# Kernel optimization log

Measured on AMD Instinct MI355X. Metric: run time of the kernel, lower is better.

The kernel has to match this reference:

```python
import jax, jax.numpy as jnp
import numpy as np

NUM_LAYERS = 4
HIDDEN = 64
IN_CH = 3
OUT_CH = 1


def setup_inputs() -> dict:
    key = jax.random.key(0)
    ks = jax.random.split(key, 16)
    s = 0.1  # weight init scale
    x = jax.random.normal(ks[0], (2, 64, 64, IN_CH), dtype=jnp.float32)
    lift_w = jax.random.normal(ks[1], (IN_CH, HIDDEN), dtype=jnp.float32) * s
    lift_b = jax.random.normal(ks[2], (HIDDEN,), dtype=jnp.float32) * s
    blk_w = jax.random.normal(ks[3], (NUM_LAYERS, HIDDEN, HIDDEN), dtype=jnp.float32) * s
    blk_b = jax.random.normal(ks[4], (NUM_LAYERS, HIDDEN), dtype=jnp.float32) * s
    q_w = jax.random.normal(ks[5], (NUM_LAYERS, HIDDEN, HIDDEN), dtype=jnp.float32) * s
    q_b = jax.random.normal(ks[6], (NUM_LAYERS, HIDDEN), dtype=jnp.float32) * s
    k_w = jax.random.normal(ks[7], (NUM_LAYERS, HIDDEN, HIDDEN), dtype=jnp.float32) * s
    k_b = jax.random.normal(ks[8], (NUM_LAYERS, HIDDEN), dtype=jnp.float32) * s
    v_w = jax.random.normal(ks[9], (NUM_LAYERS, HIDDEN, HIDDEN), dtype=jnp.float32) * s
    v_b = jax.random.normal(ks[10], (NUM_LAYERS, HIDDEN), dtype=jnp.float32) * s
    proj_w = jax.random.normal(ks[11], (HIDDEN, OUT_CH), dtype=jnp.float32) * s
    proj_b = jax.random.normal(ks[12], (OUT_CH,), dtype=jnp.float32) * s
    return {"x": x, "lift_w": lift_w, "lift_b": lift_b,
            "blk_w": blk_w, "blk_b": blk_b,
            "q_w": q_w, "q_b": q_b, "k_w": k_w, "k_b": k_b,
            "v_w": v_w, "v_b": v_b, "proj_w": proj_w, "proj_b": proj_b}


def reference(x, lift_w, lift_b, blk_w, blk_b, q_w, q_b, k_w, k_b, v_w, v_b, proj_w, proj_b):
    prefix = x.shape[:-1]           # (B, H, W)
    B = x.shape[0]
    xf = x.reshape(B, -1, x.shape[-1])   # [B, N, in_ch]
    N = xf.shape[1]
    h = xf @ lift_w + lift_b             # [B, N, d]
    d = h.shape[-1]
    scale = 1.0 / jnp.sqrt(jnp.float32(d))
    for i in range(NUM_LAYERS):
        q = h @ q_w[i] + q_b[i]
        k = h @ k_w[i] + k_b[i]
        v = h @ v_w[i] + v_b[i]
        # full dense kernel, as in torch.bmm(q, k^T)/sqrt(d)
        kern = jnp.einsum('bnd,bmd->bnm', q, k) * scale     # [B, N, N]
        integral = jnp.einsum('bnm,bmd->bnd', kern, v) / N  # [B, N, d]
        wh = h @ blk_w[i] + blk_b[i]
        h = jax.nn.gelu(wh + integral, approximate=False)   # torch F.gelu default = exact erf
    out = h @ proj_w + proj_b                               # [B, N, out_ch]
    return out.reshape(*prefix, out.shape[-1])
```

## Files before the change

### kernel.cpp

```cpp
#include <hip/hip_runtime.h>
#include <hip/hip_bf16.h>
#include <math.h>


#define NLAYER 4
#define NB 2
#define NN 4096
#define DD 64
#define RPB 32
#define NT 256
#define NBLK 256
#define SHP 68
#define C0F (1.0f/32768.0f)
#define PSZ 2304
#define NCH 128
#define CHW 18

typedef __hip_bfloat16 bf16;
typedef unsigned long long u64t;

__device__ __forceinline__ float b2f(const bf16 v) { return __bfloat162float(v); }

template <typename T> struct Acc;
template <> struct Acc<float> {
    static __device__ __forceinline__ float ld(const void* p, int i) { return ((const float*)p)[i]; }
    static __device__ __forceinline__ void st(void* p, int i, float v) { ((float*)p)[i] = v; }
};
template <> struct Acc<bf16> {
    static __device__ __forceinline__ float ld(const void* p, int i) { return b2f(((const bf16*)p)[i]); }
    static __device__ __forceinline__ void st(void* p, int i, float v) { ((bf16*)p)[i] = __float2bfloat16(v); }
};

__device__ __forceinline__ float gelu_exact(float x) {
    return 0.5f * x * (1.0f + erff(x * 0.70710678118654752f));
}

__device__ __forceinline__ float2 ldc2(const float* p) {
    u64t v = __hip_atomic_load((const u64t*)p, __ATOMIC_RELAXED, __HIP_MEMORY_SCOPE_AGENT);
    float2 r;
    r.x = __uint_as_float((unsigned)v);
    r.y = __uint_as_float((unsigned)(v >> 32));
    return r;
}
__device__ __forceinline__ void stc2(float* p, float a, float b) {
    u64t v = ((u64t)__float_as_uint(b) << 32) | (u64t)__float_as_uint(a);
    __hip_atomic_store((u64t*)p, v, __ATOMIC_RELAXED, __HIP_MEMORY_SCOPE_AGENT);
}
__device__ __forceinline__ unsigned ldw(unsigned* p) {
    return __hip_atomic_load(p, __ATOMIC_RELAXED, __HIP_MEMORY_SCOPE_AGENT);
}
__device__ __forceinline__ void stw(unsigned* p, unsigned v) {
    __hip_atomic_store(p, v, __ATOMIC_RELAXED, __HIP_MEMORY_SCOPE_AGENT);
}
__device__ __forceinline__ void pollw(unsigned* p, unsigned ep) {
    int guard = 0;
    while (ldw(p) < ep && ++guard < (1 << 18)) __builtin_amdgcn_s_sleep(2);
}

__device__ __forceinline__ void mm4x4(float (&acc)[4][4],
    float4 L0, float4 L1, float4 L2, float4 L3,
    float4 R0, float4 R1, float4 R2, float4 R3)
{
    const float L[4][4] = {{L0.x,L0.y,L0.z,L0.w},{L1.x,L1.y,L1.z,L1.w},
                           {L2.x,L2.y,L2.z,L2.w},{L3.x,L3.y,L3.z,L3.w}};
    const float R[4][4] = {{R0.x,R0.y,R0.z,R0.w},{R1.x,R1.y,R1.z,R1.w},
                           {R2.x,R2.y,R2.z,R2.w},{R3.x,R3.y,R3.z,R3.w}};
    #pragma unroll
    for (int a = 0; a < 4; a++)
        #pragma unroll
        for (int k = 0; k < 4; k++)
            #pragma unroll
            for (int b = 0; b < 4; b++)
                acc[a][b] += L[a][k] * R[k][b];
}

__device__ __forceinline__ void mmNT4x4(float (&acc)[4][4],
    float4 L0, float4 L1, float4 L2, float4 L3,
    float4 R0, float4 R1, float4 R2, float4 R3)
{
    const float L[4][4] = {{L0.x,L0.y,L0.z,L0.w},{L1.x,L1.y,L1.z,L1.w},
                           {L2.x,L2.y,L2.z,L2.w},{L3.x,L3.y,L3.z,L3.w}};
    const float R[4][4] = {{R0.x,R0.y,R0.z,R0.w},{R1.x,R1.y,R1.z,R1.w},
                           {R2.x,R2.y,R2.z,R2.w},{R3.x,R3.y,R3.z,R3.w}};
    #pragma unroll
    for (int a = 0; a < 4; a++)
        #pragma unroll
        for (int b = 0; b < 4; b++)
            #pragma unroll
            for (int k = 0; k < 4; k++)
                acc[a][b] += L[a][k] * R[b][k];
}

__device__ __forceinline__ void outer4x4(float (&acc)[4][4], float4 A, float4 B)
{
    const float Aa[4] = {A.x, A.y, A.z, A.w};
    const float Ba[4] = {B.x, B.y, B.z, B.w};
    #pragma unroll
    for (int a = 0; a < 4; a++)
        #pragma unroll
        for (int b = 0; b < 4; b++)
            acc[a][b] += Aa[a] * Ba[b];
}


#define SM_SS   23936
#define SM_SU   24000
#define SM_BK   24064
#define SM_BQ   24128
#define SM_BV   24192
#define SM_BE   24256
#define SM_QK   24320
#define SM_KQ   24384
#define SM_QBK  24448
#define SM_RED  24512
#define SM_TOT  24768

template <typename T>
__device__ void run_net(
    const void* x, const void* lw, const void* lb,
    const void* blkw, const void* blkb,
    const void* qw, const void* qb, const void* kw, const void* kb,
    const void* vw, const void* vb, const void* pw, const void* pb,
    void* out, float* Gpart, float* Gg,
    unsigned* aflag, unsigned* cflag,
    float* smem, int blk, int t)
{
    float (*sH)[SHP] = (float(*)[SHP])(smem);
    float (*B1)[SHP] = (float(*)[SHP])(smem + 2176);
    float (*B2)[SHP] = (float(*)[SHP])(smem + 6528);
    float (*B3)[SHP] = (float(*)[SHP])(smem + 10880);
    float (*B4)[SHP] = (float(*)[SHP])(smem + 15232);
    float (*B5)[SHP] = (float(*)[SHP])(smem + 19584);
    float* PS  = smem + 10880;
    float* RED = smem + 10880;
    float* sS  = smem + SM_SS;
    float* suS = smem + SM_SU;
    float* bkS = smem + SM_BK;
    float* bqS = smem + SM_BQ;
    float* bvS = smem + SM_BV;
    float* beS = smem + SM_BE;
    float* qkS = smem + SM_QK;
    float* kqS = smem + SM_KQ;
    float* qbkS = smem + SM_QBK;
    float (*red)[DD] = (float(*)[DD])(smem + SM_RED);

    const int row0 = blk * RPB;
    const int bb = blk >> 7;
    const int r = t >> 4, c4 = (t & 15) << 2;
    const int i4 = t >> 4, j4 = t & 15;
    const int r0 = i4 << 2, c0 = j4 << 2;

    #pragma unroll
    for (int a = 0; a < 2; a++) {
        const int row = r + 16 * a, gr = row0 + row;
        float x0 = Acc<T>::ld(x, gr * 3 + 0);
        float x1 = Acc<T>::ld(x, gr * 3 + 1);
        float x2 = Acc<T>::ld(x, gr * 3 + 2);
        float o[4];
        #pragma unroll
        for (int b = 0; b < 4; b++) {
            int c = c4 + b;
            o[b] = Acc<T>::ld(lb, c) + x0 * Acc<T>::ld(lw, c)
                 + x1 * Acc<T>::ld(lw, DD + c) + x2 * Acc<T>::ld(lw, 2 * DD + c);
        }
        *(float4*)&sH[row][c4] = make_float4(o[0], o[1], o[2], o[3]);
    }
    __syncthreads();

    for (int layer = 0; layer < NLAYER; layer++) {
        const unsigned ep = (unsigned)(layer + 1);
        float* GgL = Gg + (size_t)(layer * NB + bb) * PSZ;
        const int wOff = layer * DD * DD, bOff = layer * DD;

        {
            if (i4 <= j4) {
                float m[4][4];
                #pragma unroll
                for (int a = 0; a < 4; a++)
                    #pragma unroll
                    for (int b = 0; b < 4; b++) m[a][b] = 0.f;
                #pragma unroll 8
                for (int n = 0; n < RPB; n++)
                    outer4x4(m, *(const float4*)&sH[n][r0], *(const float4*)&sH[n][c0]);
                float* dst = PS + (i4 * (33 - i4) / 2 + (j4 - i4)) * 16;
                #pragma unroll
                for (int a = 0; a < 4; a++)
                    #pragma unroll
                    for (int b = 0; b < 4; b++) dst[a * 4 + b] = m[a][b];
            }
            if (t < DD) {
                float ss = 0.f;
                #pragma unroll 8
                for (int n = 0; n < RPB; n++) ss += sH[n][t];
                PS[2176 + t] = ss;
                PS[2240 + t] = 0.f;
            }
        }
        __syncthreads();
        {
            float* slot = Gpart + (size_t)blk * PSZ;
            #pragma unroll
            for (int k2 = 0; k2 < 4; k2++) {
                const int idx = 2 * (t + k2 * NT);
                stc2(&slot[idx], PS[idx], PS[idx + 1]);
            }
            if (t < 128) {
                const int idx = 2 * (t + 4 * NT);
                stc2(&slot[idx], PS[idx], PS[idx + 1]);
            }
        }
        __syncthreads();
        if (t == 0) stw(&aflag[blk], ep);

        for (int i2 = t; i2 < DD * DD; i2 += NT) {
            B1[i2 >> 6][i2 & 63] = Acc<T>::ld(qw, wOff + i2);
            B4[i2 >> 6][i2 & 63] = Acc<T>::ld(kw, wOff + i2);
        }
        if (t < DD) {
            bkS[t] = Acc<T>::ld(kb, bOff + t);
            bqS[t] = Acc<T>::ld(qb, bOff + t);
            bvS[t] = Acc<T>::ld(vb, bOff + t);
        }

        {
            if (t < NCH) pollw(&aflag[bb * NCH + t], ep);
            __syncthreads();
            const int chunk = blk & (NCH - 1);
            if (t < 144) {
                const int g = t / 9, p2 = t % 9;
                const float* base = Gpart + (size_t)(bb * NCH + g * 8) * PSZ
                                  + chunk * CHW + 2 * p2;
                float ax = 0.f, ay = 0.f;
                #pragma unroll
                for (int s2 = 0; s2 < 8; s2++) {
                    float2 v = ldc2(base + (size_t)s2 * PSZ);
                    ax += v.x; ay += v.y;
                }
                RED[g * 20 + 2 * p2]     = ax;
                RED[g * 20 + 2 * p2 + 1] = ay;
            }
            __syncthreads();
            if (t < 9) {
                float s0 = 0.f, s1 = 0.f;
                #pragma unroll
                for (int g = 0; g < 16; g++) {
                    s0 += RED[g * 20 + 2 * t];
                    s1 += RED[g * 20 + 2 * t + 1];
                }
                stc2(&GgL[chunk * CHW + 2 * t], s0, s1);
            }
            __syncthreads();
            if (t == 0) stw(&cflag[blk], ep);
        }

        {
            float acc[4][4];
            #pragma unroll
            for (int a = 0; a < 4; a++)
                #pragma unroll
                for (int b = 0; b < 4; b++) acc[a][b] = 0.f;
            #pragma unroll 2
            for (int e = 0; e < DD; e += 4)
                mmNT4x4(acc,
                      *(const float4*)&B1[r0 + 0][e], *(const float4*)&B1[r0 + 1][e],
                      *(const float4*)&B1[r0 + 2][e], *(const float4*)&B1[r0 + 3][e],
                      *(const float4*)&B4[c0 + 0][e], *(const float4*)&B4[c0 + 1][e],
                      *(const float4*)&B4[c0 + 2][e], *(const float4*)&B4[c0 + 3][e]);
            #pragma unroll
            for (int a = 0; a < 4; a++)
                *(float4*)&B2[r0 + a][c0] = make_float4(acc[a][0], acc[a][1], acc[a][2], acc[a][3]);

            if (t < DD) {
                float u = 0.f;
                for (int e = 0; e < DD; e++) u += B1[t][e] * bkS[e];
                qkS[t] = u;
            } else if (t < 2 * DD) {
                const int rr = t - DD;
                float u = 0.f;
                for (int e = 0; e < DD; e++) u += B4[rr][e] * bqS[e];
                kqS[rr] = u;
            } else if (t == 2 * DD) {
                float u = 0.f;
                for (int e = 0; e < DD; e++) u += bqS[e] * bkS[e];
                qbkS[0] = u;
            }
        }
        __syncthreads();
        for (int i2 = t; i2 < DD * DD; i2 += NT) {
            B1[i2 >> 6][i2 & 63] = Acc<T>::ld(vw, wOff + i2);
            B4[i2 >> 6][i2 & 63] = Acc<T>::ld(blkw, wOff + i2);
        }

        {
            if (t < NCH) pollw(&cflag[bb * NCH + t], ep);
            __syncthreads();
            if (i4 <= j4) {
                const float* src = GgL + (i4 * (33 - i4) / 2 + (j4 - i4)) * 16;
                #pragma unroll
                for (int a = 0; a < 4; a++)
                    *(float4*)&B3[r0 + a][c0] = *(const float4*)&src[a * 4];
            } else {
                const float* src = GgL + (j4 * (33 - j4) / 2 + (i4 - j4)) * 16;
                #pragma unroll
                for (int a = 0; a < 4; a++)
                    #pragma unroll
                    for (int b = 0; b < 4; b++)
                        B3[r0 + a][c0 + b] = src[b * 4 + a];
            }
            if (t < DD) sS[t] = GgL[2176 + t];
            __syncthreads();
        }

        {
            float acc[4][4];
            #pragma unroll
            for (int a = 0; a < 4; a++)
                #pragma unroll
                for (int b = 0; b < 4; b++) acc[a][b] = sS[r0 + a] * bvS[c0 + b];
            #pragma unroll 2
            for (int e = 0; e < DD; e += 4)
                mm4x4(acc,
                      *(const float4*)&B3[r0 + 0][e], *(const float4*)&B3[r0 + 1][e],
                      *(const float4*)&B3[r0 + 2][e], *(const float4*)&B3[r0 + 3][e],
                      *(const float4*)&B1[e + 0][c0], *(const float4*)&B1[e + 1][c0],
                      *(const float4*)&B1[e + 2][c0], *(const float4*)&B1[e + 3][c0]);
            #pragma unroll
            for (int a = 0; a < 4; a++)
                *(float4*)&B5[r0 + a][c0] = make_float4(acc[a][0], acc[a][1], acc[a][2], acc[a][3]);
        }
        {
            const int c = t & 63, q = t >> 6;
            float u = 0.f;
            #pragma unroll
            for (int d2 = 0; d2 < 16; d2++) u += sS[q * 16 + d2] * B1[q * 16 + d2][c];
            red[q][c] = u;
        }
        __syncthreads();
        if (t < DD) suS[t] = red[0][t] + red[1][t] + red[2][t] + red[3][t] + (float)NN * bvS[t];
        __syncthreads();

        {
            float acc[4][4];
            #pragma unroll
            for (int a = 0; a < 4; a++)
                #pragma unroll
                for (int b = 0; b < 4; b++) acc[a][b] = qkS[r0 + a] * suS[c0 + b];
            #pragma unroll 2
            for (int e = 0; e < DD; e += 4)
                mm4x4(acc,
                      *(const float4*)&B2[r0 + 0][e], *(const float4*)&B2[r0 + 1][e],
                      *(const float4*)&B2[r0 + 2][e], *(const float4*)&B2[r0 + 3][e],
                      *(const float4*)&B5[e + 0][c0], *(const float4*)&B5[e + 1][c0],
                      *(const float4*)&B5[e + 2][c0], *(const float4*)&B5[e + 3][c0]);
            float wloc[4][4];
            #pragma unroll
            for (int a = 0; a < 4; a++)
                #pragma unroll
                for (int b = 0; b < 4; b++)
                    wloc[a][b] = B4[r0 + a][c0 + b] + C0F * acc[a][b];
            {
                const int c = t & 63, q = t >> 6;
                float u = 0.f;
                #pragma unroll
                for (int e2 = 0; e2 < 16; e2++) u += kqS[q * 16 + e2] * B5[q * 16 + e2][c];
                red[q][c] = u;
            }
            __syncthreads();
            #pragma unroll
            for (int a = 0; a < 4; a++)
                *(float4*)&B3[r0 + a][c0] = make_float4(wloc[a][0], wloc[a][1], wloc[a][2], wloc[a][3]);
            if (t < DD) beS[t] = Acc<T>::ld(blkb, bOff + t)
                               + C0F * (red[0][t] + red[1][t] + red[2][t] + red[3][t]
                                        + qbkS[0] * suS[t]);
        }
        __syncthreads();

        float o[2][4];
        #pragma unroll
        for (int a = 0; a < 2; a++) {
            const int row = r + 16 * a;
            float acc2[4];
            #pragma unroll
            for (int b = 0; b < 4; b++) acc2[b] = beS[c4 + b];
            for (int d = 0; d < DD; d++) {
                float hv = sH[row][d];
                float4 w4 = *(const float4*)&B3[d][c4];
                acc2[0] += hv * w4.x; acc2[1] += hv * w4.y;
                acc2[2] += hv * w4.z; acc2[3] += hv * w4.w;
            }
            #pragma unroll
            for (int b = 0; b < 4; b++) o[a][b] = gelu_exact(acc2[b]);
        }

        if (layer == NLAYER - 1) {
            float pbv = Acc<T>::ld(pb, 0);
            #pragma unroll
            for (int a = 0; a < 2; a++) {
                float p = 0.f;
                #pragma unroll
                for (int b = 0; b < 4; b++) p += o[a][b] * Acc<T>::ld(pw, c4 + b);
                p += __shfl_xor(p, 1);
                p += __shfl_xor(p, 2);
                p += __shfl_xor(p, 4);
                p += __shfl_xor(p, 8);
                if ((t & 15) == 0) Acc<T>::st(out, row0 + r + 16 * a, p + pbv);
            }
        } else {
            __syncthreads();
            #pragma unroll
            for (int a = 0; a < 2; a++)
                *(float4*)&sH[r + 16 * a][c4] =
                    make_float4(o[a][0], o[a][1], o[a][2], o[a][3]);
            __syncthreads();
        }
    }
}

__global__ __launch_bounds__(NT) void gno_kernel(
    const void* x, const void* lw, const void* lb,
    const void* blkw, const void* blkb,
    const void* qw, const void* qb, const void* kw, const void* kb,
    const void* vw, const void* vb, const void* pw, const void* pb,
    void* out, float* Gpart, float* Gg, unsigned* bar, int mode)
{
    __shared__ alignas(16) float smem[SM_TOT];
    __shared__ int stot;

    const int blk = blockIdx.x, t = threadIdx.x;

    bool isbf;
    if (mode >= 0) {
        isbf = (mode == 1);
    } else {
        if (t == 0) stot = 0;
        __syncthreads();
        int cdt = 0;
        const unsigned int* xw = (const unsigned int*)x;
        for (int i = t; i < 8192; i += NT) {
            unsigned u = xw[i] & 0xFFFFu;
            int e = (u >> 7) & 0xFF;
            cdt += (u == 0u || (e >= 100 && e <= 142)) ? 1 : 0;
        }
        atomicAdd(&stot, cdt);
        __syncthreads();
        isbf = (stot > 4915);
    }

    unsigned* aflag = bar;
    unsigned* cflag = bar + 256;

    if (isbf)
        run_net<bf16>(x, lw, lb, blkw, blkb, qw, qb, kw, kb, vw, vb, pw, pb,
                      out, Gpart, Gg, aflag, cflag, smem, blk, t);
    else
        run_net<float>(x, lw, lb, blkw, blkb, qw, qb, kw, kb, vw, vb, pw, pb,
                       out, Gpart, Gg, aflag, cflag, smem, blk, t);
}

extern "C" void kernel_launch(void* const* d_in, const int* in_sizes, int n_in,
                              void* d_out, int out_size, void* d_ws, size_t ws_size,
                              hipStream_t stream)
{
    const void* x    = d_in[0];
    const void* lw   = d_in[1];
    const void* lb   = d_in[2];
    const void* blkw = d_in[3];
    const void* blkb = d_in[4];
    const void* qw   = d_in[5];
    const void* qb   = d_in[6];
    const void* kw   = d_in[7];
    const void* kb   = d_in[8];
    const void* vw   = d_in[9];
    const void* vb   = d_in[10];
    const void* pw   = d_in[11];
    const void* pb   = d_in[12];

    int mode = -1;
    if (in_sizes && n_in > 0) {
        if (in_sizes[0] == 49152) mode = 1;
        else if (in_sizes[0] == 98304) mode = 0;
    }

    unsigned* bar = (unsigned*)d_ws;
    float* Gpart  = (float*)d_ws + 512;
    float* Gg     = Gpart + (size_t)NBLK * PSZ;

    (void)hipMemsetAsync(bar, 0, 512 * sizeof(unsigned), stream);
    gno_kernel<<<NBLK, NT, 0, stream>>>(x, lw, lb, blkw, blkb, qw, qb, kw, kb,
                                        vw, vb, pw, pb, d_out, Gpart, Gg, bar, mode);
}
```

Measured before the change: 158.1 us.

## Distribute Gram reduction by rows and fold V projection into per-row reduce

Each block now writes the full 64x64 Gram partial instead of the packed upper triangle. The cross-block reduction is reassigned so 65 blocks each reduce one row (or the column sums) and immediately multiply it by Wv. This removes the per-block 64x64x64 G·Wv matmul and the symmetric unpack, since every block then reads the finished G·Wv from global memory. In exchange it nearly doubles the partial-write traffic, leaves most blocks idle during the reduction, and moves the V weight load earlier.

```diff
diff --git a/kernel.cpp b/kernel.cpp
--- a/kernel.cpp
+++ b/kernel.cpp
@@ -12,9 +12,8 @@
 #define NBLK 256
 #define SHP 68
 #define C0F (1.0f/32768.0f)
-#define PSZ 2304
+#define PSZ 4160
 #define NCH 128
-#define CHW 18
 
 typedef __hip_bfloat16 bf16;
 typedef unsigned long long u64t;
@@ -146,6 +145,7 @@
 
     const int row0 = blk * RPB;
     const int bb = blk >> 7;
+    const int RC = blk & 127;
     const int r = t >> 4, c4 = (t & 15) << 2;
     const int i4 = t >> 4, j4 = t & 15;
     const int r0 = i4 << 2, c0 = j4 << 2;
@@ -173,39 +173,34 @@
         const int wOff = layer * DD * DD, bOff = layer * DD;
 
         {
-            if (i4 <= j4) {
-                float m[4][4];
-                #pragma unroll
-                for (int a = 0; a < 4; a++)
-                    #pragma unroll
-                    for (int b = 0; b < 4; b++) m[a][b] = 0.f;
-                #pragma unroll 8
-                for (int n = 0; n < RPB; n++)
-                    outer4x4(m, *(const float4*)&sH[n][r0], *(const float4*)&sH[n][c0]);
-                float* dst = PS + (i4 * (33 - i4) / 2 + (j4 - i4)) * 16;
-                #pragma unroll
-                for (int a = 0; a < 4; a++)
-                    #pragma unroll
-                    for (int b = 0; b < 4; b++) dst[a * 4 + b] = m[a][b];
-            }
+            float m[4][4];
+            #pragma unroll
+            for (int a = 0; a < 4; a++)
+                #pragma unroll
+                for (int b = 0; b < 4; b++) m[a][b] = 0.f;
+            #pragma unroll 8
+            for (int n = 0; n < RPB; n++)
+                outer4x4(m, *(const float4*)&sH[n][r0], *(const float4*)&sH[n][c0]);
+            #pragma unroll
+            for (int a = 0; a < 4; a++)
+                *(float4*)&PS[(r0 + a) * DD + c0] = make_float4(m[a][0], m[a][1], m[a][2], m[a][3]);
             if (t < DD) {
                 float ss = 0.f;
                 #pragma unroll 8
                 for (int n = 0; n < RPB; n++) ss += sH[n][t];
-                PS[2176 + t] = ss;
-                PS[2240 + t] = 0.f;
+                PS[4096 + t] = ss;
             }
         }
         __syncthreads();
         {
             float* slot = Gpart + (size_t)blk * PSZ;
             #pragma unroll
-            for (int k2 = 0; k2 < 4; k2++) {
+            for (int k2 = 0; k2 < 8; k2++) {
                 const int idx = 2 * (t + k2 * NT);
                 stc2(&slot[idx], PS[idx], PS[idx + 1]);
             }
-            if (t < 128) {
-                const int idx = 2 * (t + 4 * NT);
+            if (t < 32) {
+                const int idx = 2 * (t + 8 * NT);
                 stc2(&slot[idx], PS[idx], PS[idx + 1]);
             }
         }
@@ -215,6 +210,7 @@
         for (int i2 = t; i2 < DD * DD; i2 += NT) {
             B1[i2 >> 6][i2 & 63] = Acc<T>::ld(qw, wOff + i2);
             B4[i2 >> 6][i2 & 63] = Acc<T>::ld(kw, wOff + i2);
+            B5[i2 >> 6][i2 & 63] = Acc<T>::ld(vw, wOff + i2);
         }
         if (t < DD) {
             bkS[t] = Acc<T>::ld(kb, bOff + t);
@@ -222,36 +218,64 @@
             bvS[t] = Acc<T>::ld(vb, bOff + t);
         }
 
-        {
+        if (RC <= 64) {
             if (t < NCH) pollw(&aflag[bb * NCH + t], ep);
             __syncthreads();
-            const int chunk = blk & (NCH - 1);
-            if (t < 144) {
-                const int g = t / 9, p2 = t % 9;
-                const float* base = Gpart + (size_t)(bb * NCH + g * 8) * PSZ
-                                  + chunk * CHW + 2 * p2;
+            const int p2 = t & 31, g8 = t >> 5;
+            const int roff = (RC < 64) ? RC * DD : 4096;
+            {
+                const float* base = Gpart + (size_t)(bb * NCH + g8 * 16) * PSZ + roff + 2 * p2;
                 float ax = 0.f, ay = 0.f;
                 #pragma unroll
-                for (int s2 = 0; s2 < 8; s2++) {
+                for (int s2 = 0; s2 < 16; s2++) {
                     float2 v = ldc2(base + (size_t)s2 * PSZ);
                     ax += v.x; ay += v.y;
                 }
-                RED[g * 20 + 2 * p2]     = ax;
-                RED[g * 20 + 2 * p2 + 1] = ay;
-            }
-            __syncthreads();
-            if (t < 9) {
-                float s0 = 0.f, s1 = 0.f;
-                #pragma unroll
-                for (int g = 0; g < 16; g++) {
-                    s0 += RED[g * 20 + 2 * t];
-                    s1 += RED[g * 20 + 2 * t + 1];
+                RED[g8 * 64 + 2 * p2]     = ax;
+                RED[g8 * 64 + 2 * p2 + 1] = ay;
+            }
+            __syncthreads();
+            if (RC < 64) {
+                if (t < DD) {
+                    float u = 0.f;
+                    #pragma unroll
+                    for (int g = 0; g < 8; g++) u += RED[g * 64 + t];
+                    RED[512 + t] = u;
                 }
-                stc2(&GgL[chunk * CHW + 2 * t], s0, s1);
+                __syncthreads();
+                {
+                    const int c = t & 63, q4 = t >> 6;
+                    float u = 0.f;
+                    #pragma unroll
+                    for (int e2 = 0; e2 < 16; e2++)
+                        u += RED[512 + q4 * 16 + e2] * B5[q4 * 16 + e2][c];
+                    RED[576 + q4 * 64 + c] = u;
+                }
+                __syncthreads();
+                if (t < 32) {
+                    float v0 = 0.f, v1 = 0.f;
+                    #pragma unroll
+                    for (int q = 0; q < 4; q++) {
+                        v0 += RED[576 + q * 64 + 2 * t];
+                        v1 += RED[576 + q * 64 + 2 * t + 1];
+                    }
+                    stc2(&GgL[RC * DD + 2 * t], v0, v1);
+                }
+            } else {
+                if (t < 32) {
+                    float v0 = 0.f, v1 = 0.f;
+                    #pragma unroll
+                    for (int g = 0; g < 8; g++) {
+                        v0 += RED[g * 64 + 2 * t];
+                        v1 += RED[g * 64 + 2 * t + 1];
+                    }
+                    stc2(&GgL[4096 + 2 * t], v0, v1);
+                }
             }
             __syncthreads();
             if (t == 0) stw(&cflag[blk], ep);
         }
+        __syncthreads();
 
         {
             float acc[4][4];
@@ -286,53 +310,31 @@
             }
         }
         __syncthreads();
-        for (int i2 = t; i2 < DD * DD; i2 += NT) {
-            B1[i2 >> 6][i2 & 63] = Acc<T>::ld(vw, wOff + i2);
+        for (int i2 = t; i2 < DD * DD; i2 += NT)
             B4[i2 >> 6][i2 & 63] = Acc<T>::ld(blkw, wOff + i2);
-        }
-
-        {
-            if (t < NCH) pollw(&cflag[bb * NCH + t], ep);
-            __syncthreads();
-            if (i4 <= j4) {
-                const float* src = GgL + (i4 * (33 - i4) / 2 + (j4 - i4)) * 16;
-                #pragma unroll
-                for (int a = 0; a < 4; a++)
-                    *(float4*)&B3[r0 + a][c0] = *(const float4*)&src[a * 4];
-            } else {
-                const float* src = GgL + (j4 * (33 - j4) / 2 + (i4 - j4)) * 16;
-                #pragma unroll
-                for (int a = 0; a < 4; a++)
-                    #pragma unroll
-                    for (int b = 0; b < 4; b++)
-                        B3[r0 + a][c0 + b] = src[b * 4 + a];
-            }
-            if (t < DD) sS[t] = GgL[2176 + t];
-            __syncthreads();
-        }
-
-        {
-            float acc[4][4];
-            #pragma unroll
-            for (int a = 0; a < 4; a++)
-                #pragma unroll
-                for (int b = 0; b < 4; b++) acc[a][b] = sS[r0 + a] * bvS[c0 + b];
-            #pragma unroll 2
-            for (int e = 0; e < DD; e += 4)
-                mm4x4(acc,
-                      *(const float4*)&B3[r0 + 0][e], *(const float4*)&B3[r0 + 1][e],
-                      *(const float4*)&B3[r0 + 2][e], *(const float4*)&B3[r0 + 3][e],
-                      *(const float4*)&B1[e + 0][c0], *(const float4*)&B1[e + 1][c0],
-                      *(const float4*)&B1[e + 2][c0], *(const float4*)&B1[e + 3][c0]);
-            #pragma unroll
-            for (int a = 0; a < 4; a++)
-                *(float4*)&B5[r0 + a][c0] = make_float4(acc[a][0], acc[a][1], acc[a][2], acc[a][3]);
-        }
+
+        {
+            if (t < 65) pollw(&cflag[bb * NCH + t], ep);
+            __syncthreads();
+            #pragma unroll
+            for (int a = 0; a < 4; a++) {
+                float4 v = *(const float4*)&GgL[(r0 + a) * DD + c0];
+                const float sv = GgL[4096 + r0 + a];
+                v.x += sv * bvS[c0 + 0];
+                v.y += sv * bvS[c0 + 1];
+                v.z += sv * bvS[c0 + 2];
+                v.w += sv * bvS[c0 + 3];
+                *(float4*)&B3[r0 + a][c0] = v;
+            }
+            if (t < DD) sS[t] = GgL[4096 + t];
+            __syncthreads();
+        }
+
         {
             const int c = t & 63, q = t >> 6;
             float u = 0.f;
             #pragma unroll
-            for (int d2 = 0; d2 < 16; d2++) u += sS[q * 16 + d2] * B1[q * 16 + d2][c];
+            for (int d2 = 0; d2 < 16; d2++) u += sS[q * 16 + d2] * B5[q * 16 + d2][c];
             red[q][c] = u;
         }
         __syncthreads();
@@ -350,25 +352,25 @@
                 mm4x4(acc,
                       *(const float4*)&B2[r0 + 0][e], *(const float4*)&B2[r0 + 1][e],
                       *(const float4*)&B2[r0 + 2][e], *(const float4*)&B2[r0 + 3][e],
-                      *(const float4*)&B5[e + 0][c0], *(const float4*)&B5[e + 1][c0],
-                      *(const float4*)&B5[e + 2][c0], *(const float4*)&B5[e + 3][c0]);
-            float wloc[4][4];
-            #pragma unroll
-            for (int a = 0; a < 4; a++)
-                #pragma unroll
-                for (int b = 0; b < 4; b++)
-                    wloc[a][b] = B4[r0 + a][c0 + b] + C0F * acc[a][b];
+                      *(const float4*)&B3[e + 0][c0], *(const float4*)&B3[e + 1][c0],
+                      *(const float4*)&B3[e + 2][c0], *(const float4*)&B3[e + 3][c0]);
+            #pragma unroll
+            for (int a = 0; a < 4; a++) {
+                float4 w;
+                w.x = B4[r0 + a][c0 + 0] + C0F * acc[a][0];
+                w.y = B4[r0 + a][c0 + 1] + C0F * acc[a][1];
+                w.z = B4[r0 + a][c0 + 2] + C0F * acc[a][2];
+                w.w = B4[r0 + a][c0 + 3] + C0F * acc[a][3];
+                *(float4*)&B5[r0 + a][c0] = w;
+            }
             {
                 const int c = t & 63, q = t >> 6;
                 float u = 0.f;
                 #pragma unroll
-                for (int e2 = 0; e2 < 16; e2++) u += kqS[q * 16 + e2] * B5[q * 16 + e2][c];
+                for (int e2 = 0; e2 < 16; e2++) u += kqS[q * 16 + e2] * B3[q * 16 + e2][c];
                 red[q][c] = u;
             }
             __syncthreads();
-            #pragma unroll
-            for (int a = 0; a < 4; a++)
-                *(float4*)&B3[r0 + a][c0] = make_float4(wloc[a][0], wloc[a][1], wloc[a][2], wloc[a][3]);
             if (t < DD) beS[t] = Acc<T>::ld(blkb, bOff + t)
                                + C0F * (red[0][t] + red[1][t] + red[2][t] + red[3][t]
                                         + qbkS[0] * suS[t]);
@@ -384,7 +386,7 @@
             for (int b = 0; b < 4; b++) acc2[b] = beS[c4 + b];
             for (int d = 0; d < DD; d++) {
                 float hv = sH[row][d];
-                float4 w4 = *(const float4*)&B3[d][c4];
+                float4 w4 = *(const float4*)&B5[d][c4];
                 acc2[0] += hv * w4.x; acc2[1] += hv * w4.y;
                 acc2[2] += hv * w4.z; acc2[3] += hv * w4.w;
             }
```

Measured after the change: 154.2 us. 2.4% less time.
